# Kernel tuning notes

Measured on AMD Instinct MI355X. Metric: run time of the kernel, lower is better.

Reference implementation:

```python
import jax, jax.numpy as jnp
import numpy as np

D_MODEL = 1024
N_HEADS = 16
HEAD_DIM = D_MODEL // N_HEADS
B, T_Q, T_CACHE = 2, 2048, 2048


def setup_inputs() -> dict:
    key = jax.random.key(0)
    ks = jax.random.split(key, 12)
    s = 1.0 / np.sqrt(D_MODEL)
    return {
        "x": jax.random.normal(ks[0], (B, T_Q, D_MODEL), jnp.float32),
        "k_cache": jax.random.normal(ks[1], (B, N_HEADS, T_CACHE, HEAD_DIM), jnp.float32),
        "v_cache": jax.random.normal(ks[2], (B, N_HEADS, T_CACHE, HEAD_DIM), jnp.float32),
        "Wq": jax.random.normal(ks[3], (D_MODEL, D_MODEL), jnp.float32) * s,
        "bq": jax.random.normal(ks[4], (D_MODEL,), jnp.float32) * s,
        "Wk": jax.random.normal(ks[5], (D_MODEL, D_MODEL), jnp.float32) * s,
        "bk": jax.random.normal(ks[6], (D_MODEL,), jnp.float32) * s,
        "Wv": jax.random.normal(ks[7], (D_MODEL, D_MODEL), jnp.float32) * s,
        "bv": jax.random.normal(ks[8], (D_MODEL,), jnp.float32) * s,
        "Wo": jax.random.normal(ks[9], (D_MODEL, D_MODEL), jnp.float32) * s,
        "bo": jax.random.normal(ks[10], (D_MODEL,), jnp.float32) * s,
    }


def reference(x, k_cache, v_cache, Wq, bq, Wk, bk, Wv, bv, Wo, bo):
    B_, T, C = x.shape
    H, Dh = N_HEADS, HEAD_DIM
    scale = Dh ** -0.5

    def proj(W, b):
        # [B,T,C] -> [B,H,T,Dh]
        y = jnp.einsum('btc,cd->btd', x, W) + b
        return y.reshape(B_, T, H, Dh).transpose(0, 2, 1, 3)

    q = proj(Wq, bq)
    k = jnp.concatenate([k_cache, proj(Wk, bk)], axis=2)
    v = jnp.concatenate([v_cache, proj(Wv, bv)], axis=2)

    Tq, Tk = q.shape[2], k.shape[2]
    scores = jnp.einsum('bhqd,bhkd->bhqk', q, k) * scale  # [B,H,Tq,Tk]
    # causal: query i attends to keys j <= i + (Tk - Tq)
    i = jnp.arange(Tq)[:, None]
    j = jnp.arange(Tk)[None, :]
    mask = j > i + (Tk - Tq)
    scores = jnp.where(mask, -jnp.inf, scores)
    attn = jax.nn.softmax(scores, axis=-1)
    out = jnp.einsum('bhqk,bhkd->bhqd', attn, v)
    out = out.transpose(0, 2, 1, 3).reshape(B_, T, C)
    out = jnp.einsum('btc,cd->btd', out, Wo) + bo
    return out, (k, v)
```

## Files before the change

### kernel.cpp

```cpp
#include <hip/hip_runtime.h>
#include <hip/hip_bf16.h>
#include <cstdint>
#include <cstddef>

#define DM 1024
#define NH 16
#define DH 64
#define BB 2
#define TQ 2048
#define TCACHE 2048
#define TKTOT 4096
#define MROWS 4096

typedef __attribute__((ext_vector_type(8))) short bf16x8;
typedef __attribute__((ext_vector_type(4))) float f32x4;
typedef __attribute__((ext_vector_type(16))) float f32x16;

__device__ __forceinline__ unsigned pk2(float a, float b) {
  unsigned r;
  asm("v_cvt_pk_bf16_f32 %0, %1, %2" : "=v"(r) : "v"(a), "v"(b));
  return r;
}

__device__ __forceinline__ short f2bf(float f) {
  return (short)(unsigned short)pk2(f, f);
}

__device__ __forceinline__ uint2 pk4(float x, float y, float z, float w) {
  uint2 r;
  r.x = pk2(x, y);
  r.y = pk2(z, w);
  return r;
}

__device__ __forceinline__ float bf2f(short s) {
  union { unsigned u; float f; } v;
  v.u = ((unsigned)(unsigned short)s) << 16;
  return v.f;
}

__device__ __forceinline__ float exp2fast(float x) {
#if __has_builtin(__builtin_amdgcn_exp2f)
  return __builtin_amdgcn_exp2f(x);
#else
  return exp2f(x);
#endif
}

__device__ __forceinline__ void plswap(unsigned& a, unsigned& b) {
  asm volatile("v_permlane32_swap_b32 %0, %1" : "+v"(a), "+v"(b));
}

__device__ __forceinline__ void gld_lds16(const short* g, short* l) {
  __builtin_amdgcn_global_load_lds(
      (const __attribute__((address_space(1))) void*)((uintptr_t)g),
      (__attribute__((address_space(3))) void*)((uintptr_t)l), 16, 0, 0);
}

__global__ __launch_bounds__(256) void k_prep(
    const float* __restrict__ x, short* __restrict__ xb,
    const float* __restrict__ W0, const float* __restrict__ W1,
    const float* __restrict__ W2, const float* __restrict__ W3,
    short* __restrict__ Wt) {
  __shared__ short lds[32 * 33];
  const int bid = (int)blockIdx.x;
  if (bid < 4096) {
    const size_t i = (size_t)bid * 256 + threadIdx.x;
    const float4 v = ((const float4*)x)[i];
    *(uint2*)(((short4*)xb) + i) = pk4(v.x, v.y, v.z, v.w);
  } else {
    const int local = bid - 4096;
    const int bx = local & 31, by = (local >> 5) & 31, bz = local >> 10;
    short (*tile)[33] = (short(*)[33])lds;
    const float* W = (bz == 0) ? W0 : (bz == 1) ? W1 : (bz == 2) ? W2 : W3;
    short* dst = Wt + (size_t)bz * DM * DM;
    const int k0 = by * 32, n0 = bx * 32;
    const int tx = threadIdx.x & 31, ty = threadIdx.x >> 5;
#pragma unroll
    for (int r = 0; r < 4; r++) {
      const int k = ty + r * 8;
      tile[k][tx] = f2bf(W[(size_t)(k0 + k) * DM + n0 + tx]);
    }
    __syncthreads();
#pragma unroll
    for (int r = 0; r < 4; r++) {
      const int n = ty + r * 8;
      dst[(size_t)(n0 + n) * DM + k0 + tx] = tile[tx][n];
    }
  }
}

__global__ __launch_bounds__(256) void k_qkv(
    const short* __restrict__ A, const short* __restrict__ Bt,
    const float* __restrict__ b0, const float* __restrict__ b1, const float* __restrict__ b2,
    short* __restrict__ Qb, short* __restrict__ Kb, short* __restrict__ Vtb,
    const float* __restrict__ kc, const float* __restrict__ vc) {
  __shared__ short SH[16384];
  const int bid = (int)blockIdx.x;
  if (bid < 768) {
    const int z = bid >> 8;
    const int by = (bid >> 3) & 31;
    const int bx = bid & 7;
    const short* Bz = Bt + (size_t)z * DM * DM;
    const float* bias = (z == 0) ? b0 : (z == 1 ? b1 : b2);

    const int m0 = by * 128;
    const int n0 = bx * 128;
    const int tid = threadIdx.x;
    const int wv = tid >> 6;
    const int lane = tid & 63;
    const int quad = lane >> 4;
    const int l16 = lane & 15;
    const int wm = (wv >> 1) * 64;
    const int wn = (wv & 1) * 64;

    const f32x4 zero = {0.f, 0.f, 0.f, 0.f};
    f32x4 acc[4][4];
#pragma unroll
    for (int i = 0; i < 4; i++)
#pragma unroll
      for (int j = 0; j < 4; j++) acc[i][j] = zero;

    const int sw = (quad ^ ((l16 >> 1) & 3)) << 4;
    const int afo = (wm + l16) * 64 + sw;
    const int bfo = (wn + l16) * 64 + sw;

#define STAGEG(k0_, b_)                                                              \
    do {                                                                             \
      _Pragma("unroll") for (int s = 0; s < 2; s++) {                                \
        const int c = tid + s * 256;                                                 \
        const int row = c >> 2, cs = c & 3;                                          \
        const int gc = cs ^ ((row >> 1) & 3);                                        \
        gld_lds16(A + (size_t)(m0 + row) * DM + (k0_) + gc * 8,                      \
                  SH + (b_) * 4096 + c * 8);                                         \
        gld_lds16(Bz + (size_t)(n0 + row) * DM + (k0_) + gc * 8,                     \
                  SH + 8192 + (b_) * 4096 + c * 8);                                  \
      }                                                                              \
    } while (0)

    STAGEG(0, 0);
    __syncthreads();
    int buf = 0;
    for (int k0 = 0; k0 < DM; k0 += 32) {
      if (k0 + 32 < DM) STAGEG(k0 + 32, buf ^ 1);
      const char* Ab = (const char*)SH + buf * 8192;
      const char* Bb = (const char*)SH + 16384 + buf * 8192;
      bf16x8 af[4], bfv[4];
#pragma unroll
      for (int i = 0; i < 4; i++) af[i] = *(const bf16x8*)(Ab + afo + i * 1024);
#pragma unroll
      for (int j = 0; j < 4; j++) bfv[j] = *(const bf16x8*)(Bb + bfo + j * 1024);
      __builtin_amdgcn_s_setprio(1);
#pragma unroll
      for (int i = 0; i < 4; i++)
#pragma unroll
        for (int j = 0; j < 4; j++)
          acc[i][j] = __builtin_amdgcn_mfma_f32_16x16x32_bf16(af[i], bfv[j], acc[i][j], 0, 0, 0);
      __builtin_amdgcn_s_setprio(0);
      __syncthreads();
      buf ^= 1;
    }
#undef STAGEG

#pragma unroll
    for (int i = 0; i < 4; i++) {
#pragma unroll
      for (int j = 0; j < 4; j++) {
        const int gn = n0 + wn + j * 16 + l16;
        const float bb = bias[gn];
#pragma unroll
        for (int r = 0; r < 4; r++) {
          const int gm = m0 + wm + i * 16 + quad * 4 + r;
          const float v = acc[i][j][r] + bb;
          const int b_ = gm >> 11, t = gm & 2047;
          const int h_ = gn >> 6, dh = gn & 63;
          if (z == 0) {
            Qb[(((size_t)(b_ * NH + h_)) * TQ + t) * DH + dh] = f2bf(v * 0.18033688011f);
          } else if (z == 1) {
            Kb[(((size_t)(b_ * NH + h_)) * TKTOT + TCACHE + t) * DH + dh] = f2bf(v);
          } else {
            Vtb[(((size_t)(b_ * NH + h_)) * DH + dh) * TKTOT + TCACHE + t] = f2bf(v);
          }
        }
      }
    }
  } else if (bid < 4864) {
    const size_t i = (size_t)(bid - 768) * 256 + threadIdx.x;
    const float4 v = ((const float4*)kc)[i];
    const size_t e = i * 4;
    const int dh = (int)(e & 63);
    const int t = (int)((e >> 6) & 2047);
    const int bh = (int)(e >> 17);
    *(uint2*)(Kb + ((size_t)bh * TKTOT + t) * DH + dh) = pk4(v.x, v.y, v.z, v.w);
  } else {
    const int local = bid - 4864;
    const int bh = local >> 5;
    const int t0 = (local & 31) * 64;
    short (*tile)[65] = (short(*)[65])SH;
    const int tx = threadIdx.x & 15, ty = threadIdx.x >> 4;
    const float* src = vc + ((size_t)bh * TCACHE + t0) * DH;
#pragma unroll
    for (int r = 0; r < 4; r++) {
      const int t = ty + r * 16;
      const float4 v = *(const float4*)(src + (size_t)t * DH + tx * 4);
      tile[tx * 4 + 0][t] = f2bf(v.x);
      tile[tx * 4 + 1][t] = f2bf(v.y);
      tile[tx * 4 + 2][t] = f2bf(v.z);
      tile[tx * 4 + 3][t] = f2bf(v.w);
    }
    __syncthreads();
    short* vt = Vtb + (size_t)bh * DH * TKTOT + t0;
#pragma unroll
    for (int r = 0; r < 4; r++) {
      const int dh = ty + r * 16;
      short4 o;
      o.x = tile[dh][tx * 4 + 0];
      o.y = tile[dh][tx * 4 + 1];
      o.z = tile[dh][tx * 4 + 2];
      o.w = tile[dh][tx * 4 + 3];
      *(short4*)(vt + (size_t)dh * TKTOT + tx * 4) = o;
    }
  }
}

__global__ __launch_bounds__(256) void k_proj(
    const short* __restrict__ A, const short* __restrict__ Bt,
    const float* __restrict__ bias, float* __restrict__ fdst) {
  __shared__ short sA[2][64 * 32];
  __shared__ short sB[2][128 * 32];

  const int m0 = blockIdx.y * 64;
  const int n0 = blockIdx.x * 128;
  const int tid = threadIdx.x;
  const int wv = tid >> 6;
  const int lane = tid & 63;
  const int quad = lane >> 4;
  const int l16 = lane & 15;
  const int wm = (wv >> 1) * 32;
  const int wn = (wv & 1) * 64;

  const f32x4 zero = {0.f, 0.f, 0.f, 0.f};
  f32x4 acc[2][4];
#pragma unroll
  for (int i = 0; i < 2; i++)
#pragma unroll
    for (int j = 0; j < 4; j++) acc[i][j] = zero;

  const int sw = (quad ^ ((l16 >> 1) & 3)) << 4;
  const int afo = (wm + l16) * 64 + sw;
  const int bfo = (wn + l16) * 64 + sw;

#define STAGEP(k0_, b_)                                                          \
  do {                                                                           \
    {                                                                            \
      const int c = tid;                                                         \
      const int row = c >> 2, cs = c & 3;                                        \
      const int gc = cs ^ ((row >> 1) & 3);                                      \
      gld_lds16(A + (size_t)(m0 + row) * DM + (k0_) + gc * 8, &sA[b_][c * 8]);   \
    }                                                                            \
    _Pragma("unroll") for (int s = 0; s < 2; s++) {                              \
      const int c = tid + s * 256;                                               \
      const int row = c >> 2, cs = c & 3;                                        \
      const int gc = cs ^ ((row >> 1) & 3);                                      \
      gld_lds16(Bt + (size_t)(n0 + row) * DM + (k0_) + gc * 8, &sB[b_][c * 8]);  \
    }                                                                            \
  } while (0)

  STAGEP(0, 0);
  __syncthreads();
  int buf = 0;
  for (int k0 = 0; k0 < DM; k0 += 32) {
    if (k0 + 32 < DM) STAGEP(k0 + 32, buf ^ 1);
    const char* Ab = (const char*)&sA[0][0] + buf * 4096;
    const char* Bb = (const char*)&sB[0][0] + buf * 8192;
    bf16x8 af[2], bfv[4];
#pragma unroll
    for (int i = 0; i < 2; i++) af[i] = *(const bf16x8*)(Ab + afo + i * 1024);
#pragma unroll
    for (int j = 0; j < 4; j++) bfv[j] = *(const bf16x8*)(Bb + bfo + j * 1024);
    __builtin_amdgcn_s_setprio(1);
#pragma unroll
    for (int i = 0; i < 2; i++)
#pragma unroll
      for (int j = 0; j < 4; j++)
        acc[i][j] = __builtin_amdgcn_mfma_f32_16x16x32_bf16(af[i], bfv[j], acc[i][j], 0, 0, 0);
    __builtin_amdgcn_s_setprio(0);
    __syncthreads();
    buf ^= 1;
  }
#undef STAGEP

#pragma unroll
  for (int i = 0; i < 2; i++) {
#pragma unroll
    for (int j = 0; j < 4; j++) {
      const int gn = n0 + wn + j * 16 + l16;
      const float bb = bias[gn];
#pragma unroll
      for (int r = 0; r < 4; r++) {
        const int gm = m0 + wm + i * 16 + quad * 4 + r;
        fdst[(size_t)gm * DM + gn] = acc[i][j][r] + bb;
      }
    }
  }
}

__global__ __launch_bounds__(256, 4) void k_attn_expand(
    const short* __restrict__ Qb, const short* __restrict__ Kb,
    const short* __restrict__ Vtb, short* __restrict__ AOb,
    const float* __restrict__ kc, float* __restrict__ kF,
    const float* __restrict__ vc, float* __restrict__ vF) {
  __shared__ short SH[16384];

  const int bid = (int)blockIdx.x;
  if (bid < 512) {
    const int y = bid >> 5;
    const int bh = bid & 31;
    const int qx = (y < 8) ? (15 - y) : (y - 8);
    const int q0 = qx * 128;
    const int tid = threadIdx.x;
    const int wq = tid >> 6;
    const int lane = tid & 63;
    const int l32 = lane & 31;
    const int h = lane >> 5;

    const int nkt = 2 * qx + 34;

    const short* Kg = Kb + (size_t)bh * TKTOT * DH;
    const short* Vtg = Vtb + (size_t)bh * DH * TKTOT;

    const int c0 = tid, c1 = tid + 256;
    const int r0 = c0 >> 3, g0 = ((c0 & 7) ^ (r0 & 7)) * 8;
    const int r1 = c1 >> 3, g1 = ((c1 & 7) ^ (r1 & 7)) * 8;
    const short* Kst0 = Kg + (size_t)r0 * DH + g0;
    const short* Kst1 = Kg + (size_t)r1 * DH + g1;
    const short* Vst0 = Vtg + (size_t)r0 * TKTOT + g0;
    const short* Vst1 = Vtg + (size_t)r1 * TKTOT + g1;

    const short* Qrow = Qb + ((size_t)bh * TQ + q0 + wq * 32 + l32) * DH;
    bf16x8 qf[4];
#pragma unroll
    for (int s = 0; s < 4; s++) qf[s] = *(const bf16x8*)(Qrow + s * 16 + h * 8);

    const char* sKc = (const char*)SH;
    const char* sVc = (const char*)SH + 16384;
    const int rx7 = l32 & 7;
    const int base0 = l32 * 128;
    const int base1 = base0 + 4096;
    int co[4];
#pragma unroll
    for (int ks = 0; ks < 4; ks++) co[ks] = ((2 * ks + h) ^ rx7) << 4;

    const f32x16 zerov = {0, 0, 0, 0, 0, 0, 0, 0, 0, 0, 0, 0, 0, 0, 0, 0};
    f32x16 of0 = zerov;
    f32x16 of1 = zerov;
    float la = 0.f, lb = 0.f, lc = 0.f, ld = 0.f;

#define STAGE(t_, b_)                                    \
    do {                                                 \
      const size_t koff = (size_t)(t_) * 64 * DH;        \
      const size_t voff = (size_t)(t_) * 64;             \
      short* dK = SH + (b_)*4096;                        \
      short* dV = SH + 8192 + (b_)*4096;                 \
      gld_lds16(Kst0 + koff, dK + c0 * 8);               \
      gld_lds16(Kst1 + koff, dK + c1 * 8);               \
      gld_lds16(Vst0 + voff, dV + c0 * 8);               \
      gld_lds16(Vst1 + voff, dV + c1 * 8);               \
    } while (0)

    STAGE(0, 0);
    __syncthreads();
    int buf = 0;

    for (int t = 0; t < nkt; t++) {
      if (t + 1 < nkt) STAGE(t + 1, buf ^ 1);
      const char* kb_ = sKc + buf * 8192;
      const char* vb_ = sVc + buf * 8192;

      f32x16 sacc0, sacc1;
      __builtin_amdgcn_s_setprio(1);
      {
        const bf16x8 kf0 = *(const bf16x8*)(kb_ + base0 + co[0]);
        const bf16x8 kf1 = *(const bf16x8*)(kb_ + base1 + co[0]);
        sacc0 = __builtin_amdgcn_mfma_f32_32x32x16_bf16(kf0, qf[0], zerov, 0, 0, 0);
        sacc1 = __builtin_amdgcn_mfma_f32_32x32x16_bf16(kf1, qf[0], zerov, 0, 0, 0);
      }
#pragma unroll
      for (int ks = 1; ks < 4; ks++) {
        const bf16x8 kf0 = *(const bf16x8*)(kb_ + base0 + co[ks]);
        const bf16x8 kf1 = *(const bf16x8*)(kb_ + base1 + co[ks]);
        sacc0 = __builtin_amdgcn_mfma_f32_32x32x16_bf16(kf0, qf[ks], sacc0, 0, 0, 0);
        sacc1 = __builtin_amdgcn_mfma_f32_32x32x16_bf16(kf1, qf[ks], sacc1, 0, 0, 0);
      }
      __builtin_amdgcn_s_setprio(0);

      if (t >= nkt - 2) {
        const int qgl = q0 + wq * 32 + l32 + TCACHE;
        const int kb0 = t * 64 + 4 * h;
#pragma unroll
        for (int r = 0; r < 16; r++) {
          const int key = kb0 + (r & 3) + 8 * (r >> 2);
          if (key > qgl) sacc0[r] = -1e30f;
          if (key + 32 > qgl) sacc1[r] = -1e30f;
        }
      }
#pragma unroll
      for (int r = 0; r < 16; r++) {
        const float e0 = exp2fast(sacc0[r]);
        const float e1 = exp2fast(sacc1[r]);
        sacc0[r] = e0;
        sacc1[r] = e1;
        if ((r & 3) == 0) la += e0 + e1;
        else if ((r & 3) == 1) lb += e0 + e1;
        else if ((r & 3) == 2) lc += e0 + e1;
        else ld += e0 + e1;
      }

      bf16x8 pa[4];
#pragma unroll
      for (int s = 0; s < 4; s++) {
        const int o = (s & 1) * 8;
        unsigned w0, w1, w2, w3;
        if (s < 2) {
          w0 = pk2(sacc0[o + 0], sacc0[o + 1]);
          w1 = pk2(sacc0[o + 2], sacc0[o + 3]);
          w2 = pk2(sacc0[o + 4], sacc0[o + 5]);
          w3 = pk2(sacc0[o + 6], sacc0[o + 7]);
        } else {
          w0 = pk2(sacc1[o + 0], sacc1[o + 1]);
          w1 = pk2(sacc1[o + 2], sacc1[o + 3]);
          w2 = pk2(sacc1[o + 4], sacc1[o + 5]);
          w3 = pk2(sacc1[o + 6], sacc1[o + 7]);
        }
        plswap(w0, w2);
        plswap(w1, w3);
        union { unsigned u[4]; bf16x8 v; } pu;
        pu.u[0] = w0; pu.u[1] = w1; pu.u[2] = w2; pu.u[3] = w3;
        pa[s] = pu.v;
      }

      __builtin_amdgcn_s_setprio(1);
#pragma unroll
      for (int ks = 0; ks < 4; ks++) {
        const bf16x8 vf0 = *(const bf16x8*)(vb_ + base0 + co[ks]);
        const bf16x8 vf1 = *(const bf16x8*)(vb_ + base1 + co[ks]);
        of0 = __builtin_amdgcn_mfma_f32_32x32x16_bf16(pa[ks], vf0, of0, 0, 0, 0);
        of1 = __builtin_amdgcn_mfma_f32_32x32x16_bf16(pa[ks], vf1, of1, 0, 0, 0);
      }
      __builtin_amdgcn_s_setprio(0);
      __syncthreads();
      buf ^= 1;
    }
#undef STAGE

    float* sLf = (float*)SH;
    const float l_lane = (la + lb) + (lc + ld);
    const float l_tot = l_lane + __shfl_xor(l_lane, 32);
    if (h == 0) sLf[wq * 32 + l32] = l_tot;
    const int b_ = bh >> 4, h_ = bh & 15;
#pragma unroll
    for (int r = 0; r < 16; r++) {
      const int row = (r & 3) + 8 * (r >> 2) + 4 * h;
      const float inv = 1.f / sLf[wq * 32 + row];
      const int qg = q0 + wq * 32 + row;
      short* d = AOb + ((size_t)(b_ * TQ + qg)) * DM + h_ * 64;
      d[l32] = f2bf(of0[r] * inv);
      d[32 + l32] = f2bf(of1[r] * inv);
    }
  } else if (bid < 8704) {
    const size_t f4 = (size_t)(bid - 512) * 256 + threadIdx.x;
    const size_t e = f4 * 4;
    const int t = (int)((e >> 6) & 4095);
    float4 v;
    if (t < TCACHE) {
      const int dh = (int)(e & 63);
      const int bh = (int)(e >> 18);
      v = *(const float4*)(kc + ((size_t)(bh * TCACHE + t)) * DH + dh);
    } else {
      const short4 s = *(const short4*)(Kb + e);
      v.x = bf2f(s.x); v.y = bf2f(s.y); v.z = bf2f(s.z); v.w = bf2f(s.w);
    }
    *(float4*)(kF + e) = v;
  } else {
    const int local = bid - 8704;
    const int tt = local & 63, bh = local >> 6;
    short* tile = SH;
    if (tt < 32) {
#pragma unroll
      for (int k2 = 0; k2 < 4; k2++) {
        const int f = threadIdx.x + k2 * 256;
        const int trow = f >> 4, dh4 = f & 15;
        const size_t si = ((size_t)(bh * TCACHE) + tt * 64 + trow) * DH + dh4 * 4;
        const size_t di = ((size_t)(bh * TKTOT) + tt * 64 + trow) * DH + dh4 * 4;
        *(float4*)(vF + di) = *(const float4*)(vc + si);
      }
    } else {
      const int t0 = tt * 64;
#pragma unroll
      for (int k2 = 0; k2 < 4; k2++) {
        const int f = threadIdx.x + k2 * 256;
        const int dh = f >> 4, tc4 = f & 15;
        const short4 s = *(const short4*)(Vtb + ((size_t)(bh * DH + dh)) * TKTOT + t0 + tc4 * 4);
        *(short4*)(&tile[dh * 72 + tc4 * 4]) = s;
      }
      __syncthreads();
#pragma unroll
      for (int k2 = 0; k2 < 4; k2++) {
        const int f = threadIdx.x + k2 * 256;
        const int trow = f >> 4, dh4 = f & 15;
        float4 v;
        v.x = bf2f(tile[(dh4 * 4 + 0) * 72 + trow]);
        v.y = bf2f(tile[(dh4 * 4 + 1) * 72 + trow]);
        v.z = bf2f(tile[(dh4 * 4 + 2) * 72 + trow]);
        v.w = bf2f(tile[(dh4 * 4 + 3) * 72 + trow]);
        *(float4*)(vF + ((size_t)(bh * TKTOT) + t0 + trow) * DH + dh4 * 4) = v;
      }
    }
  }
}


extern "C" void kernel_launch(void* const* d_in, const int* in_sizes, int n_in,
                              void* d_out, int out_size, void* d_ws, size_t ws_size,
                              hipStream_t stream) {
  const float* x = (const float*)d_in[0];
  const float* kc = (const float*)d_in[1];
  const float* vc = (const float*)d_in[2];
  const float* Wq = (const float*)d_in[3];
  const float* bq = (const float*)d_in[4];
  const float* Wk = (const float*)d_in[5];
  const float* bk = (const float*)d_in[6];
  const float* Wv = (const float*)d_in[7];
  const float* bv = (const float*)d_in[8];
  const float* Wo = (const float*)d_in[9];
  const float* bo = (const float*)d_in[10];

  float* out = (float*)d_out;
  float* kF = out + (size_t)BB * TQ * DM;
  float* vF = kF + (size_t)BB * NH * TKTOT * DH;

  char* ws = (char*)d_ws;
  short* xb = (short*)ws;   ws += (size_t)MROWS * DM * 2;
  short* Wt = (short*)ws;   ws += (size_t)4 * DM * DM * 2;
  short* Qb = (short*)ws;   ws += (size_t)BB * NH * TQ * DH * 2;
  short* Kb = (short*)ws;   ws += (size_t)BB * NH * TKTOT * DH * 2;
  short* Vtb = (short*)ws;  ws += (size_t)BB * NH * TKTOT * DH * 2;
  short* AOb = (short*)ws;

  k_prep<<<8192, 256, 0, stream>>>(x, xb, Wq, Wk, Wv, Wo, Wt);
  k_qkv<<<5888, 256, 0, stream>>>(xb, Wt, bq, bk, bv, Qb, Kb, Vtb, kc, vc);
  k_attn_expand<<<10752, 256, 0, stream>>>(Qb, Kb, Vtb, AOb, kc, kF, vc, vF);
  k_proj<<<dim3(8, 64), 256, 0, stream>>>(AOb, Wt + (size_t)3 * DM * DM, bo, out);
}
```

Baseline: 271.1 us.

## Split attention KV loop across two warp groups and regroup cache conversion stages

Attention now runs 512-thread blocks in which two 256-thread groups each process half of the key tiles. This is meant to cut the serial KV loop length per block and improve balance across causal tiles, at the cost of a cross-group merge step through shared memory. The fp32 K/V cache copies to the outputs move into the prep kernel, fused with the bf16 conversion so the cache is read only once. The new-token K/V expansion now rides alongside the output projection rather than the attention kernel, which leaves attention running on its own.

```diff
diff --git a/kernel.cpp b/kernel.cpp
--- a/kernel.cpp
+++ b/kernel.cpp
@@ -61,14 +61,16 @@
     const float* __restrict__ x, short* __restrict__ xb,
     const float* __restrict__ W0, const float* __restrict__ W1,
     const float* __restrict__ W2, const float* __restrict__ W3,
-    short* __restrict__ Wt) {
-  __shared__ short lds[32 * 33];
+    short* __restrict__ Wt,
+    const float* __restrict__ kc, short* __restrict__ Kb, float* __restrict__ kF,
+    const float* __restrict__ vc, short* __restrict__ Vtb, float* __restrict__ vF) {
+  __shared__ short lds[64 * 65];
   const int bid = (int)blockIdx.x;
   if (bid < 4096) {
     const size_t i = (size_t)bid * 256 + threadIdx.x;
     const float4 v = ((const float4*)x)[i];
     *(uint2*)(((short4*)xb) + i) = pk4(v.x, v.y, v.z, v.w);
-  } else {
+  } else if (bid < 8192) {
     const int local = bid - 4096;
     const int bx = local & 31, by = (local >> 5) & 31, bz = local >> 10;
     short (*tile)[33] = (short(*)[33])lds;
@@ -87,122 +89,28 @@
       const int n = ty + r * 8;
       dst[(size_t)(n0 + n) * DM + k0 + tx] = tile[tx][n];
     }
-  }
-}
-
-__global__ __launch_bounds__(256) void k_qkv(
-    const short* __restrict__ A, const short* __restrict__ Bt,
-    const float* __restrict__ b0, const float* __restrict__ b1, const float* __restrict__ b2,
-    short* __restrict__ Qb, short* __restrict__ Kb, short* __restrict__ Vtb,
-    const float* __restrict__ kc, const float* __restrict__ vc) {
-  __shared__ short SH[16384];
-  const int bid = (int)blockIdx.x;
-  if (bid < 768) {
-    const int z = bid >> 8;
-    const int by = (bid >> 3) & 31;
-    const int bx = bid & 7;
-    const short* Bz = Bt + (size_t)z * DM * DM;
-    const float* bias = (z == 0) ? b0 : (z == 1 ? b1 : b2);
-
-    const int m0 = by * 128;
-    const int n0 = bx * 128;
-    const int tid = threadIdx.x;
-    const int wv = tid >> 6;
-    const int lane = tid & 63;
-    const int quad = lane >> 4;
-    const int l16 = lane & 15;
-    const int wm = (wv >> 1) * 64;
-    const int wn = (wv & 1) * 64;
-
-    const f32x4 zero = {0.f, 0.f, 0.f, 0.f};
-    f32x4 acc[4][4];
-#pragma unroll
-    for (int i = 0; i < 4; i++)
-#pragma unroll
-      for (int j = 0; j < 4; j++) acc[i][j] = zero;
-
-    const int sw = (quad ^ ((l16 >> 1) & 3)) << 4;
-    const int afo = (wm + l16) * 64 + sw;
-    const int bfo = (wn + l16) * 64 + sw;
-
-#define STAGEG(k0_, b_)                                                              \
-    do {                                                                             \
-      _Pragma("unroll") for (int s = 0; s < 2; s++) {                                \
-        const int c = tid + s * 256;                                                 \
-        const int row = c >> 2, cs = c & 3;                                          \
-        const int gc = cs ^ ((row >> 1) & 3);                                        \
-        gld_lds16(A + (size_t)(m0 + row) * DM + (k0_) + gc * 8,                      \
-                  SH + (b_) * 4096 + c * 8);                                         \
-        gld_lds16(Bz + (size_t)(n0 + row) * DM + (k0_) + gc * 8,                     \
-                  SH + 8192 + (b_) * 4096 + c * 8);                                  \
-      }                                                                              \
-    } while (0)
-
-    STAGEG(0, 0);
-    __syncthreads();
-    int buf = 0;
-    for (int k0 = 0; k0 < DM; k0 += 32) {
-      if (k0 + 32 < DM) STAGEG(k0 + 32, buf ^ 1);
-      const char* Ab = (const char*)SH + buf * 8192;
-      const char* Bb = (const char*)SH + 16384 + buf * 8192;
-      bf16x8 af[4], bfv[4];
-#pragma unroll
-      for (int i = 0; i < 4; i++) af[i] = *(const bf16x8*)(Ab + afo + i * 1024);
-#pragma unroll
-      for (int j = 0; j < 4; j++) bfv[j] = *(const bf16x8*)(Bb + bfo + j * 1024);
-      __builtin_amdgcn_s_setprio(1);
-#pragma unroll
-      for (int i = 0; i < 4; i++)
-#pragma unroll
-        for (int j = 0; j < 4; j++)
-          acc[i][j] = __builtin_amdgcn_mfma_f32_16x16x32_bf16(af[i], bfv[j], acc[i][j], 0, 0, 0);
-      __builtin_amdgcn_s_setprio(0);
-      __syncthreads();
-      buf ^= 1;
-    }
-#undef STAGEG
-
-#pragma unroll
-    for (int i = 0; i < 4; i++) {
-#pragma unroll
-      for (int j = 0; j < 4; j++) {
-        const int gn = n0 + wn + j * 16 + l16;
-        const float bb = bias[gn];
-#pragma unroll
-        for (int r = 0; r < 4; r++) {
-          const int gm = m0 + wm + i * 16 + quad * 4 + r;
-          const float v = acc[i][j][r] + bb;
-          const int b_ = gm >> 11, t = gm & 2047;
-          const int h_ = gn >> 6, dh = gn & 63;
-          if (z == 0) {
-            Qb[(((size_t)(b_ * NH + h_)) * TQ + t) * DH + dh] = f2bf(v * 0.18033688011f);
-          } else if (z == 1) {
-            Kb[(((size_t)(b_ * NH + h_)) * TKTOT + TCACHE + t) * DH + dh] = f2bf(v);
-          } else {
-            Vtb[(((size_t)(b_ * NH + h_)) * DH + dh) * TKTOT + TCACHE + t] = f2bf(v);
-          }
-        }
-      }
-    }
-  } else if (bid < 4864) {
-    const size_t i = (size_t)(bid - 768) * 256 + threadIdx.x;
+  } else if (bid < 12288) {
+    const size_t i = (size_t)(bid - 8192) * 256 + threadIdx.x;
     const float4 v = ((const float4*)kc)[i];
     const size_t e = i * 4;
     const int dh = (int)(e & 63);
     const int t = (int)((e >> 6) & 2047);
     const int bh = (int)(e >> 17);
-    *(uint2*)(Kb + ((size_t)bh * TKTOT + t) * DH + dh) = pk4(v.x, v.y, v.z, v.w);
+    const size_t d = ((size_t)bh * TKTOT + t) * DH + dh;
+    *(uint2*)(Kb + d) = pk4(v.x, v.y, v.z, v.w);
+    *(float4*)(kF + d) = v;
   } else {
-    const int local = bid - 4864;
+    const int local = bid - 12288;
     const int bh = local >> 5;
     const int t0 = (local & 31) * 64;
-    short (*tile)[65] = (short(*)[65])SH;
+    short (*tile)[65] = (short(*)[65])lds;
     const int tx = threadIdx.x & 15, ty = threadIdx.x >> 4;
     const float* src = vc + ((size_t)bh * TCACHE + t0) * DH;
 #pragma unroll
     for (int r = 0; r < 4; r++) {
       const int t = ty + r * 16;
       const float4 v = *(const float4*)(src + (size_t)t * DH + tx * 4);
+      *(float4*)(vF + ((size_t)bh * TKTOT + t0 + t) * DH + tx * 4) = v;
       tile[tx * 4 + 0][t] = f2bf(v.x);
       tile[tx * 4 + 1][t] = f2bf(v.y);
       tile[tx * 4 + 2][t] = f2bf(v.z);
@@ -223,26 +131,30 @@
   }
 }
 
-__global__ __launch_bounds__(256) void k_proj(
+__global__ __launch_bounds__(256) void k_qkv(
     const short* __restrict__ A, const short* __restrict__ Bt,
-    const float* __restrict__ bias, float* __restrict__ fdst) {
-  __shared__ short sA[2][64 * 32];
+    const float* __restrict__ b0, const float* __restrict__ b1, const float* __restrict__ b2,
+    short* __restrict__ Qb, short* __restrict__ Kb, short* __restrict__ Vtb) {
+  __shared__ short sA[2][128 * 32];
   __shared__ short sB[2][128 * 32];
-
-  const int m0 = blockIdx.y * 64;
+  const int z = (int)blockIdx.z;
+  const short* Bz = Bt + (size_t)z * DM * DM;
+  const float* bias = (z == 0) ? b0 : (z == 1 ? b1 : b2);
+
+  const int m0 = blockIdx.y * 128;
   const int n0 = blockIdx.x * 128;
   const int tid = threadIdx.x;
   const int wv = tid >> 6;
   const int lane = tid & 63;
   const int quad = lane >> 4;
   const int l16 = lane & 15;
-  const int wm = (wv >> 1) * 32;
+  const int wm = (wv >> 1) * 64;
   const int wn = (wv & 1) * 64;
 
   const f32x4 zero = {0.f, 0.f, 0.f, 0.f};
-  f32x4 acc[2][4];
-#pragma unroll
-  for (int i = 0; i < 2; i++)
+  f32x4 acc[4][4];
+#pragma unroll
+  for (int i = 0; i < 4; i++)
 #pragma unroll
     for (int j = 0; j < 4; j++) acc[i][j] = zero;
 
@@ -250,37 +162,32 @@
   const int afo = (wm + l16) * 64 + sw;
   const int bfo = (wn + l16) * 64 + sw;
 
-#define STAGEP(k0_, b_)                                                          \
-  do {                                                                           \
-    {                                                                            \
-      const int c = tid;                                                         \
-      const int row = c >> 2, cs = c & 3;                                        \
-      const int gc = cs ^ ((row >> 1) & 3);                                      \
-      gld_lds16(A + (size_t)(m0 + row) * DM + (k0_) + gc * 8, &sA[b_][c * 8]);   \
-    }                                                                            \
-    _Pragma("unroll") for (int s = 0; s < 2; s++) {                              \
-      const int c = tid + s * 256;                                               \
-      const int row = c >> 2, cs = c & 3;                                        \
-      const int gc = cs ^ ((row >> 1) & 3);                                      \
-      gld_lds16(Bt + (size_t)(n0 + row) * DM + (k0_) + gc * 8, &sB[b_][c * 8]);  \
-    }                                                                            \
+#define STAGEG(k0_, b_)                                                         \
+  do {                                                                          \
+    _Pragma("unroll") for (int s = 0; s < 2; s++) {                             \
+      const int c = tid + s * 256;                                              \
+      const int row = c >> 2, cs = c & 3;                                       \
+      const int gc = cs ^ ((row >> 1) & 3);                                     \
+      gld_lds16(A + (size_t)(m0 + row) * DM + (k0_) + gc * 8, &sA[b_][c * 8]);  \
+      gld_lds16(Bz + (size_t)(n0 + row) * DM + (k0_) + gc * 8, &sB[b_][c * 8]); \
+    }                                                                           \
   } while (0)
 
-  STAGEP(0, 0);
+  STAGEG(0, 0);
   __syncthreads();
   int buf = 0;
   for (int k0 = 0; k0 < DM; k0 += 32) {
-    if (k0 + 32 < DM) STAGEP(k0 + 32, buf ^ 1);
-    const char* Ab = (const char*)&sA[0][0] + buf * 4096;
+    if (k0 + 32 < DM) STAGEG(k0 + 32, buf ^ 1);
+    const char* Ab = (const char*)&sA[0][0] + buf * 8192;
     const char* Bb = (const char*)&sB[0][0] + buf * 8192;
-    bf16x8 af[2], bfv[4];
-#pragma unroll
-    for (int i = 0; i < 2; i++) af[i] = *(const bf16x8*)(Ab + afo + i * 1024);
+    bf16x8 af[4], bfv[4];
+#pragma unroll
+    for (int i = 0; i < 4; i++) af[i] = *(const bf16x8*)(Ab + afo + i * 1024);
 #pragma unroll
     for (int j = 0; j < 4; j++) bfv[j] = *(const bf16x8*)(Bb + bfo + j * 1024);
     __builtin_amdgcn_s_setprio(1);
 #pragma unroll
-    for (int i = 0; i < 2; i++)
+    for (int i = 0; i < 4; i++)
 #pragma unroll
       for (int j = 0; j < 4; j++)
         acc[i][j] = __builtin_amdgcn_mfma_f32_16x16x32_bf16(af[i], bfv[j], acc[i][j], 0, 0, 0);
@@ -288,10 +195,10 @@
     __syncthreads();
     buf ^= 1;
   }
-#undef STAGEP
-
-#pragma unroll
-  for (int i = 0; i < 2; i++) {
+#undef STAGEG
+
+#pragma unroll
+  for (int i = 0; i < 4; i++) {
 #pragma unroll
     for (int j = 0; j < 4; j++) {
       const int gn = n0 + wn + j * 16 + l16;
@@ -299,222 +206,322 @@
 #pragma unroll
       for (int r = 0; r < 4; r++) {
         const int gm = m0 + wm + i * 16 + quad * 4 + r;
-        fdst[(size_t)gm * DM + gn] = acc[i][j][r] + bb;
+        const float v = acc[i][j][r] + bb;
+        const int b_ = gm >> 11, t = gm & 2047;
+        const int h_ = gn >> 6, dh = gn & 63;
+        if (z == 0) {
+          Qb[(((size_t)(b_ * NH + h_)) * TQ + t) * DH + dh] = f2bf(v * 0.18033688011f);
+        } else if (z == 1) {
+          Kb[(((size_t)(b_ * NH + h_)) * TKTOT + TCACHE + t) * DH + dh] = f2bf(v);
+        } else {
+          Vtb[(((size_t)(b_ * NH + h_)) * DH + dh) * TKTOT + TCACHE + t] = f2bf(v);
+        }
       }
     }
   }
 }
 
-__global__ __launch_bounds__(256, 4) void k_attn_expand(
+__global__ __launch_bounds__(512, 4) void k_attn(
     const short* __restrict__ Qb, const short* __restrict__ Kb,
-    const short* __restrict__ Vtb, short* __restrict__ AOb,
-    const float* __restrict__ kc, float* __restrict__ kF,
-    const float* __restrict__ vc, float* __restrict__ vF) {
-  __shared__ short SH[16384];
-
+    const short* __restrict__ Vtb, short* __restrict__ AOb) {
+  __shared__ short SH[32768];
+
+  const int bid = (int)blockIdx.x;
+  const int y = bid >> 5;
+  const int bh = bid & 31;
+  const int qx = (y < 8) ? (15 - y) : (y - 8);
+  const int q0 = qx * 128;
+  const int tid = threadIdx.x;
+  const int g = tid >> 8;
+  const int wq = (tid >> 6) & 3;
+  const int lane = tid & 63;
+  const int l32 = lane & 31;
+  const int h = lane >> 5;
+
+  const int nkt = 2 * qx + 34;
+  const int cnt = nkt >> 1;
+  const int t0g = g * cnt;
+
+  const short* Kg = Kb + (size_t)bh * TKTOT * DH;
+  const short* Vtg = Vtb + (size_t)bh * DH * TKTOT;
+
+  const int ltid = tid & 255;
+  const int c0 = ltid, c1 = ltid + 256;
+  const int r0 = c0 >> 3, g0 = ((c0 & 7) ^ (r0 & 7)) * 8;
+  const int r1 = c1 >> 3, g1 = ((c1 & 7) ^ (r1 & 7)) * 8;
+  const short* Kst0 = Kg + (size_t)r0 * DH + g0;
+  const short* Kst1 = Kg + (size_t)r1 * DH + g1;
+  const short* Vst0 = Vtg + (size_t)r0 * TKTOT + g0;
+  const short* Vst1 = Vtg + (size_t)r1 * TKTOT + g1;
+
+  char* sKbase = (char*)SH + g * 16384;
+  char* sVbase = (char*)SH + 32768 + g * 16384;
+
+  const short* Qrow = Qb + ((size_t)bh * TQ + q0 + wq * 32 + l32) * DH;
+  bf16x8 qf[4];
+#pragma unroll
+  for (int s = 0; s < 4; s++) qf[s] = *(const bf16x8*)(Qrow + s * 16 + h * 8);
+
+  const int rx7 = l32 & 7;
+  const int base0 = l32 * 128;
+  const int base1 = base0 + 4096;
+  int co[4];
+#pragma unroll
+  for (int ks = 0; ks < 4; ks++) co[ks] = ((2 * ks + h) ^ rx7) << 4;
+
+  const f32x16 zerov = {0, 0, 0, 0, 0, 0, 0, 0, 0, 0, 0, 0, 0, 0, 0, 0};
+  f32x16 of0 = zerov;
+  f32x16 of1 = zerov;
+  float la = 0.f, lb = 0.f, lc = 0.f, ld = 0.f;
+
+#define STAGE(t_, b_)                                    \
+  do {                                                   \
+    const size_t koff = (size_t)(t_) * (64 * DH);        \
+    const size_t voff = (size_t)(t_) * 64;               \
+    short* dK = (short*)(sKbase + (b_) * 8192);          \
+    short* dV = (short*)(sVbase + (b_) * 8192);          \
+    gld_lds16(Kst0 + koff, dK + c0 * 8);                 \
+    gld_lds16(Kst1 + koff, dK + c1 * 8);                 \
+    gld_lds16(Vst0 + voff, dV + c0 * 8);                 \
+    gld_lds16(Vst1 + voff, dV + c1 * 8);                 \
+  } while (0)
+
+  STAGE(t0g, 0);
+  __syncthreads();
+  int buf = 0;
+
+  for (int i = 0; i < cnt; i++) {
+    const int t = t0g + i;
+    if (i + 1 < cnt) STAGE(t + 1, buf ^ 1);
+    const char* kb_ = sKbase + buf * 8192;
+    const char* vb_ = sVbase + buf * 8192;
+
+    f32x16 sacc0, sacc1;
+    __builtin_amdgcn_s_setprio(1);
+    {
+      const bf16x8 kf0 = *(const bf16x8*)(kb_ + base0 + co[0]);
+      const bf16x8 kf1 = *(const bf16x8*)(kb_ + base1 + co[0]);
+      sacc0 = __builtin_amdgcn_mfma_f32_32x32x16_bf16(kf0, qf[0], zerov, 0, 0, 0);
+      sacc1 = __builtin_amdgcn_mfma_f32_32x32x16_bf16(kf1, qf[0], zerov, 0, 0, 0);
+    }
+#pragma unroll
+    for (int ks = 1; ks < 4; ks++) {
+      const bf16x8 kf0 = *(const bf16x8*)(kb_ + base0 + co[ks]);
+      const bf16x8 kf1 = *(const bf16x8*)(kb_ + base1 + co[ks]);
+      sacc0 = __builtin_amdgcn_mfma_f32_32x32x16_bf16(kf0, qf[ks], sacc0, 0, 0, 0);
+      sacc1 = __builtin_amdgcn_mfma_f32_32x32x16_bf16(kf1, qf[ks], sacc1, 0, 0, 0);
+    }
+    __builtin_amdgcn_s_setprio(0);
+
+    if (t >= nkt - 2) {
+      const int qgl = q0 + wq * 32 + l32 + TCACHE;
+      const int kb0 = t * 64 + 4 * h;
+#pragma unroll
+      for (int r = 0; r < 16; r++) {
+        const int key = kb0 + (r & 3) + 8 * (r >> 2);
+        if (key > qgl) sacc0[r] = -1e30f;
+        if (key + 32 > qgl) sacc1[r] = -1e30f;
+      }
+    }
+#pragma unroll
+    for (int r = 0; r < 16; r++) {
+      const float e0 = exp2fast(sacc0[r]);
+      const float e1 = exp2fast(sacc1[r]);
+      sacc0[r] = e0;
+      sacc1[r] = e1;
+      if ((r & 3) == 0) la += e0 + e1;
+      else if ((r & 3) == 1) lb += e0 + e1;
+      else if ((r & 3) == 2) lc += e0 + e1;
+      else ld += e0 + e1;
+    }
+
+    bf16x8 pa[4];
+#pragma unroll
+    for (int s = 0; s < 4; s++) {
+      const int o = (s & 1) * 8;
+      unsigned w0, w1, w2, w3;
+      if (s < 2) {
+        w0 = pk2(sacc0[o + 0], sacc0[o + 1]);
+        w1 = pk2(sacc0[o + 2], sacc0[o + 3]);
+        w2 = pk2(sacc0[o + 4], sacc0[o + 5]);
+        w3 = pk2(sacc0[o + 6], sacc0[o + 7]);
+      } else {
+        w0 = pk2(sacc1[o + 0], sacc1[o + 1]);
+        w1 = pk2(sacc1[o + 2], sacc1[o + 3]);
+        w2 = pk2(sacc1[o + 4], sacc1[o + 5]);
+        w3 = pk2(sacc1[o + 6], sacc1[o + 7]);
+      }
+      plswap(w0, w2);
+      plswap(w1, w3);
+      union { unsigned u[4]; bf16x8 v; } pu;
+      pu.u[0] = w0; pu.u[1] = w1; pu.u[2] = w2; pu.u[3] = w3;
+      pa[s] = pu.v;
+    }
+
+    __builtin_amdgcn_s_setprio(1);
+#pragma unroll
+    for (int ks = 0; ks < 4; ks++) {
+      const bf16x8 vf0 = *(const bf16x8*)(vb_ + base0 + co[ks]);
+      const bf16x8 vf1 = *(const bf16x8*)(vb_ + base1 + co[ks]);
+      of0 = __builtin_amdgcn_mfma_f32_32x32x16_bf16(pa[ks], vf0, of0, 0, 0, 0);
+      of1 = __builtin_amdgcn_mfma_f32_32x32x16_bf16(pa[ks], vf1, of1, 0, 0, 0);
+    }
+    __builtin_amdgcn_s_setprio(0);
+    __syncthreads();
+    buf ^= 1;
+  }
+#undef STAGE
+
+  float* sO = (float*)SH;
+  float* sL = (float*)((char*)SH + 32768);
+  const float l_lane = (la + lb) + (lc + ld);
+  const float l_half = l_lane + __shfl_xor(l_lane, 32);
+  if (h == 0) sL[g * 128 + wq * 32 + l32] = l_half;
+  if (g == 1) {
+    float* Op = sO + wq * 2048;
+#pragma unroll
+    for (int r = 0; r < 16; r++) {
+      const int row = (r & 3) + 8 * (r >> 2) + 4 * h;
+      Op[row * 64 + l32] = of0[r];
+      Op[row * 64 + 32 + l32] = of1[r];
+    }
+  }
+  __syncthreads();
+  if (g == 0) {
+    const float* Op = sO + wq * 2048;
+    const int b_ = bh >> 4, h_ = bh & 15;
+#pragma unroll
+    for (int r = 0; r < 16; r++) {
+      const int row = (r & 3) + 8 * (r >> 2) + 4 * h;
+      const int qrow = wq * 32 + row;
+      const float inv = 1.f / (sL[qrow] + sL[128 + qrow]);
+      const float o0 = of0[r] + Op[row * 64 + l32];
+      const float o1 = of1[r] + Op[row * 64 + 32 + l32];
+      const int qg = q0 + qrow;
+      short* d = AOb + ((size_t)(b_ * TQ + qg)) * DM + h_ * 64;
+      d[l32] = f2bf(o0 * inv);
+      d[32 + l32] = f2bf(o1 * inv);
+    }
+  }
+}
+
+__global__ __launch_bounds__(256) void k_proj_expand(
+    const short* __restrict__ A, const short* __restrict__ Bt,
+    const float* __restrict__ bias, float* __restrict__ fdst,
+    const short* __restrict__ Kb, float* __restrict__ kF,
+    const short* __restrict__ Vtb, float* __restrict__ vF) {
+  __shared__ short SH[12288];
   const int bid = (int)blockIdx.x;
   if (bid < 512) {
-    const int y = bid >> 5;
-    const int bh = bid & 31;
-    const int qx = (y < 8) ? (15 - y) : (y - 8);
-    const int q0 = qx * 128;
+    const int m0 = (bid >> 3) * 64;
+    const int n0 = (bid & 7) * 128;
     const int tid = threadIdx.x;
-    const int wq = tid >> 6;
+    const int wv = tid >> 6;
     const int lane = tid & 63;
-    const int l32 = lane & 31;
-    const int h = lane >> 5;
-
-    const int nkt = 2 * qx + 34;
-
-    const short* Kg = Kb + (size_t)bh * TKTOT * DH;
-    const short* Vtg = Vtb + (size_t)bh * DH * TKTOT;
-
-    const int c0 = tid, c1 = tid + 256;
-    const int r0 = c0 >> 3, g0 = ((c0 & 7) ^ (r0 & 7)) * 8;
-    const int r1 = c1 >> 3, g1 = ((c1 & 7) ^ (r1 & 7)) * 8;
-    const short* Kst0 = Kg + (size_t)r0 * DH + g0;
-    const short* Kst1 = Kg + (size_t)r1 * DH + g1;
-    const short* Vst0 = Vtg + (size_t)r0 * TKTOT + g0;
-    const short* Vst1 = Vtg + (size_t)r1 * TKTOT + g1;
-
-    const short* Qrow = Qb + ((size_t)bh * TQ + q0 + wq * 32 + l32) * DH;
-    bf16x8 qf[4];
-#pragma unroll
-    for (int s = 0; s < 4; s++) qf[s] = *(const bf16x8*)(Qrow + s * 16 + h * 8);
-
-    const char* sKc = (const char*)SH;
-    const char* sVc = (const char*)SH + 16384;
-    const int rx7 = l32 & 7;
-    const int base0 = l32 * 128;
-    const int base1 = base0 + 4096;
-    int co[4];
-#pragma unroll
-    for (int ks = 0; ks < 4; ks++) co[ks] = ((2 * ks + h) ^ rx7) << 4;
-
-    const f32x16 zerov = {0, 0, 0, 0, 0, 0, 0, 0, 0, 0, 0, 0, 0, 0, 0, 0};
-    f32x16 of0 = zerov;
-    f32x16 of1 = zerov;
-    float la = 0.f, lb = 0.f, lc = 0.f, ld = 0.f;
-
-#define STAGE(t_, b_)                                    \
-    do {                                                 \
-      const size_t koff = (size_t)(t_) * 64 * DH;        \
-      const size_t voff = (size_t)(t_) * 64;             \
-      short* dK = SH + (b_)*4096;                        \
-      short* dV = SH + 8192 + (b_)*4096;                 \
-      gld_lds16(Kst0 + koff, dK + c0 * 8);               \
-      gld_lds16(Kst1 + koff, dK + c1 * 8);               \
-      gld_lds16(Vst0 + voff, dV + c0 * 8);               \
-      gld_lds16(Vst1 + voff, dV + c1 * 8);               \
+    const int quad = lane >> 4;
+    const int l16 = lane & 15;
+    const int wm = (wv >> 1) * 32;
+    const int wn = (wv & 1) * 64;
+
+    const f32x4 zero = {0.f, 0.f, 0.f, 0.f};
+    f32x4 acc[2][4];
+#pragma unroll
+    for (int i = 0; i < 2; i++)
+#pragma unroll
+      for (int j = 0; j < 4; j++) acc[i][j] = zero;
+
+    const int sw = (quad ^ ((l16 >> 1) & 3)) << 4;
+    const int afo = (wm + l16) * 64 + sw;
+    const int bfo = (wn + l16) * 64 + sw;
+    char* SHb = (char*)SH;
+
+#define STAGEP(k0_, b_)                                                          \
+    do {                                                                         \
+      {                                                                          \
+        const int c = tid;                                                       \
+        const int row = c >> 2, cs = c & 3;                                      \
+        const int gc = cs ^ ((row >> 1) & 3);                                    \
+        gld_lds16(A + (size_t)(m0 + row) * DM + (k0_) + gc * 8,                  \
+                  (short*)(SHb + (b_) * 4096) + c * 8);                          \
+      }                                                                          \
+      _Pragma("unroll") for (int s = 0; s < 2; s++) {                            \
+        const int c = tid + s * 256;                                             \
+        const int row = c >> 2, cs = c & 3;                                      \
+        const int gc = cs ^ ((row >> 1) & 3);                                    \
+        gld_lds16(Bt + (size_t)(n0 + row) * DM + (k0_) + gc * 8,                 \
+                  (short*)(SHb + 8192 + (b_) * 8192) + c * 8);                   \
+      }                                                                          \
     } while (0)
 
-    STAGE(0, 0);
+    STAGEP(0, 0);
     __syncthreads();
     int buf = 0;
-
-    for (int t = 0; t < nkt; t++) {
-      if (t + 1 < nkt) STAGE(t + 1, buf ^ 1);
-      const char* kb_ = sKc + buf * 8192;
-      const char* vb_ = sVc + buf * 8192;
-
-      f32x16 sacc0, sacc1;
+    for (int k0 = 0; k0 < DM; k0 += 32) {
+      if (k0 + 32 < DM) STAGEP(k0 + 32, buf ^ 1);
+      const char* Ab = SHb + buf * 4096;
+      const char* Bb = SHb + 8192 + buf * 8192;
+      bf16x8 af[2], bfv[4];
+#pragma unroll
+      for (int i = 0; i < 2; i++) af[i] = *(const bf16x8*)(Ab + afo + i * 1024);
+#pragma unroll
+      for (int j = 0; j < 4; j++) bfv[j] = *(const bf16x8*)(Bb + bfo + j * 1024);
       __builtin_amdgcn_s_setprio(1);
-      {
-        const bf16x8 kf0 = *(const bf16x8*)(kb_ + base0 + co[0]);
-        const bf16x8 kf1 = *(const bf16x8*)(kb_ + base1 + co[0]);
-        sacc0 = __builtin_amdgcn_mfma_f32_32x32x16_bf16(kf0, qf[0], zerov, 0, 0, 0);
-        sacc1 = __builtin_amdgcn_mfma_f32_32x32x16_bf16(kf1, qf[0], zerov, 0, 0, 0);
-      }
-#pragma unroll
-      for (int ks = 1; ks < 4; ks++) {
-        const bf16x8 kf0 = *(const bf16x8*)(kb_ + base0 + co[ks]);
-        const bf16x8 kf1 = *(const bf16x8*)(kb_ + base1 + co[ks]);
-        sacc0 = __builtin_amdgcn_mfma_f32_32x32x16_bf16(kf0, qf[ks], sacc0, 0, 0, 0);
-        sacc1 = __builtin_amdgcn_mfma_f32_32x32x16_bf16(kf1, qf[ks], sacc1, 0, 0, 0);
-      }
-      __builtin_amdgcn_s_setprio(0);
-
-      if (t >= nkt - 2) {
-        const int qgl = q0 + wq * 32 + l32 + TCACHE;
-        const int kb0 = t * 64 + 4 * h;
-#pragma unroll
-        for (int r = 0; r < 16; r++) {
-          const int key = kb0 + (r & 3) + 8 * (r >> 2);
-          if (key > qgl) sacc0[r] = -1e30f;
-          if (key + 32 > qgl) sacc1[r] = -1e30f;
-        }
-      }
-#pragma unroll
-      for (int r = 0; r < 16; r++) {
-        const float e0 = exp2fast(sacc0[r]);
-        const float e1 = exp2fast(sacc1[r]);
-        sacc0[r] = e0;
-        sacc1[r] = e1;
-        if ((r & 3) == 0) la += e0 + e1;
-        else if ((r & 3) == 1) lb += e0 + e1;
-        else if ((r & 3) == 2) lc += e0 + e1;
-        else ld += e0 + e1;
-      }
-
-      bf16x8 pa[4];
-#pragma unroll
-      for (int s = 0; s < 4; s++) {
-        const int o = (s & 1) * 8;
-        unsigned w0, w1, w2, w3;
-        if (s < 2) {
-          w0 = pk2(sacc0[o + 0], sacc0[o + 1]);
-          w1 = pk2(sacc0[o + 2], sacc0[o + 3]);
-          w2 = pk2(sacc0[o + 4], sacc0[o + 5]);
-          w3 = pk2(sacc0[o + 6], sacc0[o + 7]);
-        } else {
-          w0 = pk2(sacc1[o + 0], sacc1[o + 1]);
-          w1 = pk2(sacc1[o + 2], sacc1[o + 3]);
-          w2 = pk2(sacc1[o + 4], sacc1[o + 5]);
-          w3 = pk2(sacc1[o + 6], sacc1[o + 7]);
-        }
-        plswap(w0, w2);
-        plswap(w1, w3);
-        union { unsigned u[4]; bf16x8 v; } pu;
-        pu.u[0] = w0; pu.u[1] = w1; pu.u[2] = w2; pu.u[3] = w3;
-        pa[s] = pu.v;
-      }
-
-      __builtin_amdgcn_s_setprio(1);
-#pragma unroll
-      for (int ks = 0; ks < 4; ks++) {
-        const bf16x8 vf0 = *(const bf16x8*)(vb_ + base0 + co[ks]);
-        const bf16x8 vf1 = *(const bf16x8*)(vb_ + base1 + co[ks]);
-        of0 = __builtin_amdgcn_mfma_f32_32x32x16_bf16(pa[ks], vf0, of0, 0, 0, 0);
-        of1 = __builtin_amdgcn_mfma_f32_32x32x16_bf16(pa[ks], vf1, of1, 0, 0, 0);
-      }
+#pragma unroll
+      for (int i = 0; i < 2; i++)
+#pragma unroll
+        for (int j = 0; j < 4; j++)
+          acc[i][j] = __builtin_amdgcn_mfma_f32_16x16x32_bf16(af[i], bfv[j], acc[i][j], 0, 0, 0);
       __builtin_amdgcn_s_setprio(0);
       __syncthreads();
       buf ^= 1;
     }
-#undef STAGE
-
-    float* sLf = (float*)SH;
-    const float l_lane = (la + lb) + (lc + ld);
-    const float l_tot = l_lane + __shfl_xor(l_lane, 32);
-    if (h == 0) sLf[wq * 32 + l32] = l_tot;
-    const int b_ = bh >> 4, h_ = bh & 15;
-#pragma unroll
-    for (int r = 0; r < 16; r++) {
-      const int row = (r & 3) + 8 * (r >> 2) + 4 * h;
-      const float inv = 1.f / sLf[wq * 32 + row];
-      const int qg = q0 + wq * 32 + row;
-      short* d = AOb + ((size_t)(b_ * TQ + qg)) * DM + h_ * 64;
-      d[l32] = f2bf(of0[r] * inv);
-      d[32 + l32] = f2bf(of1[r] * inv);
-    }
-  } else if (bid < 8704) {
-    const size_t f4 = (size_t)(bid - 512) * 256 + threadIdx.x;
-    const size_t e = f4 * 4;
-    const int t = (int)((e >> 6) & 4095);
+#undef STAGEP
+
+#pragma unroll
+    for (int i = 0; i < 2; i++) {
+#pragma unroll
+      for (int j = 0; j < 4; j++) {
+        const int gn = n0 + wn + j * 16 + l16;
+        const float bb = bias[gn];
+#pragma unroll
+        for (int r = 0; r < 4; r++) {
+          const int gm = m0 + wm + i * 16 + quad * 4 + r;
+          fdst[(size_t)gm * DM + gn] = acc[i][j][r] + bb;
+        }
+      }
+    }
+  } else if (bid < 4608) {
+    const int local = bid - 512;
+    const int bh = local >> 7, sub = local & 127;
+    const size_t e = ((size_t)bh * TKTOT + TCACHE) * DH +
+                     ((size_t)(sub * 256 + threadIdx.x)) * 4;
+    const short4 s = *(const short4*)(Kb + e);
     float4 v;
-    if (t < TCACHE) {
-      const int dh = (int)(e & 63);
-      const int bh = (int)(e >> 18);
-      v = *(const float4*)(kc + ((size_t)(bh * TCACHE + t)) * DH + dh);
-    } else {
-      const short4 s = *(const short4*)(Kb + e);
-      v.x = bf2f(s.x); v.y = bf2f(s.y); v.z = bf2f(s.z); v.w = bf2f(s.w);
-    }
+    v.x = bf2f(s.x); v.y = bf2f(s.y); v.z = bf2f(s.z); v.w = bf2f(s.w);
     *(float4*)(kF + e) = v;
   } else {
-    const int local = bid - 8704;
-    const int tt = local & 63, bh = local >> 6;
+    const int local = bid - 4608;
+    const int bh = local >> 5;
+    const int t0 = TCACHE + (local & 31) * 64;
     short* tile = SH;
-    if (tt < 32) {
-#pragma unroll
-      for (int k2 = 0; k2 < 4; k2++) {
-        const int f = threadIdx.x + k2 * 256;
-        const int trow = f >> 4, dh4 = f & 15;
-        const size_t si = ((size_t)(bh * TCACHE) + tt * 64 + trow) * DH + dh4 * 4;
-        const size_t di = ((size_t)(bh * TKTOT) + tt * 64 + trow) * DH + dh4 * 4;
-        *(float4*)(vF + di) = *(const float4*)(vc + si);
-      }
-    } else {
-      const int t0 = tt * 64;
-#pragma unroll
-      for (int k2 = 0; k2 < 4; k2++) {
-        const int f = threadIdx.x + k2 * 256;
-        const int dh = f >> 4, tc4 = f & 15;
-        const short4 s = *(const short4*)(Vtb + ((size_t)(bh * DH + dh)) * TKTOT + t0 + tc4 * 4);
-        *(short4*)(&tile[dh * 72 + tc4 * 4]) = s;
-      }
-      __syncthreads();
-#pragma unroll
-      for (int k2 = 0; k2 < 4; k2++) {
-        const int f = threadIdx.x + k2 * 256;
-        const int trow = f >> 4, dh4 = f & 15;
-        float4 v;
-        v.x = bf2f(tile[(dh4 * 4 + 0) * 72 + trow]);
-        v.y = bf2f(tile[(dh4 * 4 + 1) * 72 + trow]);
-        v.z = bf2f(tile[(dh4 * 4 + 2) * 72 + trow]);
-        v.w = bf2f(tile[(dh4 * 4 + 3) * 72 + trow]);
-        *(float4*)(vF + ((size_t)(bh * TKTOT) + t0 + trow) * DH + dh4 * 4) = v;
-      }
+#pragma unroll
+    for (int k2 = 0; k2 < 4; k2++) {
+      const int f = threadIdx.x + k2 * 256;
+      const int dh = f >> 4, tc4 = f & 15;
+      const short4 s = *(const short4*)(Vtb + ((size_t)(bh * DH + dh)) * TKTOT + t0 + tc4 * 4);
+      *(short4*)(&tile[dh * 72 + tc4 * 4]) = s;
+    }
+    __syncthreads();
+#pragma unroll
+    for (int k2 = 0; k2 < 4; k2++) {
+      const int f = threadIdx.x + k2 * 256;
+      const int trow = f >> 4, dh4 = f & 15;
+      float4 v;
+      v.x = bf2f(tile[(dh4 * 4 + 0) * 72 + trow]);
+      v.y = bf2f(tile[(dh4 * 4 + 1) * 72 + trow]);
+      v.z = bf2f(tile[(dh4 * 4 + 2) * 72 + trow]);
+      v.w = bf2f(tile[(dh4 * 4 + 3) * 72 + trow]);
+      *(float4*)(vF + ((size_t)(bh * TKTOT) + t0 + trow) * DH + dh4 * 4) = v;
     }
   }
 }
@@ -547,8 +554,9 @@
   short* Vtb = (short*)ws;  ws += (size_t)BB * NH * TKTOT * DH * 2;
   short* AOb = (short*)ws;
 
-  k_prep<<<8192, 256, 0, stream>>>(x, xb, Wq, Wk, Wv, Wo, Wt);
-  k_qkv<<<5888, 256, 0, stream>>>(xb, Wt, bq, bk, bv, Qb, Kb, Vtb, kc, vc);
-  k_attn_expand<<<10752, 256, 0, stream>>>(Qb, Kb, Vtb, AOb, kc, kF, vc, vF);
-  k_proj<<<dim3(8, 64), 256, 0, stream>>>(AOb, Wt + (size_t)3 * DM * DM, bo, out);
-}
+  k_prep<<<13312, 256, 0, stream>>>(x, xb, Wq, Wk, Wv, Wo, Wt, kc, Kb, kF, vc, Vtb, vF);
+  k_qkv<<<dim3(8, 32, 3), 256, 0, stream>>>(xb, Wt, bq, bk, bv, Qb, Kb, Vtb);
+  k_attn<<<512, 512, 0, stream>>>(Qb, Kb, Vtb, AOb);
+  k_proj_expand<<<5632, 256, 0, stream>>>(AOb, Wt + (size_t)3 * DM * DM, bo, out,
+                                          Kb, kF, Vtb, vF);
+}
```

New measurement: 277.0 us. +2.2%, slower.
